# Optimization experiments

Hardware: AMD Instinct MI355X
Metric: run time of the kernel (lower is better)

Reference implementation:

```python
import jax, jax.numpy as jnp
import numpy as np

B, C, H, W = 32, 3, 128, 128
NMIX = 10  # 10 logistic mixture components -> 100 param channels for RGB


def setup_inputs() -> dict:
    key = jax.random.key(0)
    k1, k2 = jax.random.split(key)
    samples = jax.random.uniform(k1, (B, C, H, W), dtype=jnp.float32)  # pixel values in [0,1]
    params = jax.random.normal(k2, (B, 10 * NMIX, H, W), dtype=jnp.float32)  # PixelCNN output params
    return {"samples": samples, "params": params}


def _discretized_mix_logistic_log_prob(x, l):
    # x: [B,H,W,3] in [-1,1]; l: [B,H,W,100]
    logit_probs = l[..., :NMIX]                                   # [B,H,W,NMIX]
    rest = l[..., NMIX:].reshape(l.shape[0], l.shape[1], l.shape[2], 3, 3 * NMIX)
    means = rest[..., :NMIX]                                      # [B,H,W,3,NMIX]
    log_scales = jnp.maximum(rest[..., NMIX:2 * NMIX], -7.0)
    coeffs = jnp.tanh(rest[..., 2 * NMIX:3 * NMIX])

    x0 = x[..., 0:1]  # [B,H,W,1]
    x1 = x[..., 1:2]
    m1 = means[..., 0, :]
    m2 = means[..., 1, :] + coeffs[..., 0, :] * x0
    m3 = means[..., 2, :] + coeffs[..., 1, :] * x0 + coeffs[..., 2, :] * x1
    means_c = jnp.stack([m1, m2, m3], axis=3)                     # [B,H,W,3,NMIX]

    xb = x[..., None]                                             # [B,H,W,3,1]
    centered = xb - means_c
    inv_stdv = jnp.exp(-log_scales)
    plus_in = inv_stdv * (centered + 1.0 / 255.0)
    min_in = inv_stdv * (centered - 1.0 / 255.0)
    cdf_plus = jax.nn.sigmoid(plus_in)
    cdf_min = jax.nn.sigmoid(min_in)
    log_cdf_plus = plus_in - jax.nn.softplus(plus_in)             # log CDF at left edge bin (x = -1)
    log_one_minus_cdf_min = -jax.nn.softplus(min_in)              # log(1-CDF) at right edge bin (x = 1)
    cdf_delta = cdf_plus - cdf_min
    mid_in = inv_stdv * centered
    log_pdf_mid = mid_in - log_scales - 2.0 * jax.nn.softplus(mid_in)

    inner = jnp.where(cdf_delta > 1e-5,
                      jnp.log(jnp.maximum(cdf_delta, 1e-12)),
                      log_pdf_mid - np.float32(np.log(127.5)))
    log_probs_ch = jnp.where(xb < -0.999, log_cdf_plus,
                             jnp.where(xb > 0.999, log_one_minus_cdf_min, inner))
    # sum over channels, mixture weights, logsumexp over mixtures
    log_probs = log_probs_ch.sum(axis=3) + jax.nn.log_softmax(logit_probs, axis=-1)
    return jax.scipy.special.logsumexp(log_probs, axis=-1).sum()


def reference(samples, params):
    # _PixelCNNDistribution.log_prob: rescale samples to [-1,1], evaluate
    # discretized mixture-of-logistics log-likelihood (= -discretized_mix_logistic_loss).
    x = jnp.transpose(samples * 2.0 - 1.0, (0, 2, 3, 1))  # NCHW -> NHWC
    l = jnp.transpose(params, (0, 2, 3, 1))
    return _discretized_mix_logistic_log_prob(x, l)
```

## Files before the change

### kernel.cpp

```cpp
#include <hip/hip_runtime.h>
#include <math.h>

#define HW 16384
#define HW2 8192
#define NMIX 10
#define NPIX (32 * HW)
#define NTHREADS (NPIX / 2)
#define NBLOCKS (NTHREADS / 256)

__device__ __forceinline__ float fexp(float x) { return __expf(x); }
__device__ __forceinline__ float flog(float x) { return __logf(x); }
__device__ __forceinline__ float frcp(float x) { return __builtin_amdgcn_rcpf(x); }

__device__ __forceinline__ float ftanh(float y) {
    float t = fexp(-2.0f * fabsf(y));
    float r = (1.0f - t) * frcp(1.0f + t);
    return (y >= 0.0f) ? r : -r;
}

__device__ __forceinline__ float channel_logprob(float x, float mean, float ls,
                                                 bool waveEdge) {
    const float INV255 = 0.00392156862745098f;
    const float LOG127_5 = 4.852030263919617f;
    float inv = fexp(-ls);
    float centered = x - mean;
    float plus_in = inv * (centered + INV255);
    float min_in  = inv * (centered - INV255);
    float mid_in  = inv * centered;

    float tp = fexp(-fabsf(plus_in));
    float rp = frcp(1.0f + tp);
    float sig_plus = (plus_in >= 0.0f) ? rp : tp * rp;

    float tm = fexp(-fabsf(min_in));
    float rm = frcp(1.0f + tm);
    float sig_min = (min_in >= 0.0f) ? rm : tm * rm;

    float cdf_delta = sig_plus - sig_min;

    float tmid = fexp(-fabsf(mid_in));
    float sp_mid = fmaxf(mid_in, 0.0f) + flog(1.0f + tmid);
    float log_pdf_mid = mid_in - ls - 2.0f * sp_mid;

    float r = (cdf_delta > 1e-5f) ? flog(fmaxf(cdf_delta, 1e-12f))
                                  : (log_pdf_mid - LOG127_5);
    if (waveEdge) {
        float sp_plus = fmaxf(plus_in, 0.0f) + flog(1.0f + tp);
        float sp_min  = fmaxf(min_in, 0.0f) + flog(1.0f + tm);
        float log_cdf_plus   = plus_in - sp_plus;
        float log_om_cdf_min = -sp_min;
        r = (x < -0.999f) ? log_cdf_plus
          : ((x > 0.999f) ? log_om_cdf_min : r);
    }
    return r;
}

__device__ __forceinline__ void lse_update(float& m, float& s, float v) {
    float d = v - m;
    float e = fexp(-fabsf(d));
    bool grow = (d > 0.0f);
    s = grow ? (s * e + 1.0f) : (s + e);
    m = grow ? v : m;
}

__global__ __launch_bounds__(256, 6) void pixelcnn_kernel(
    const float2* __restrict__ samples, const float2* __restrict__ params,
    float* __restrict__ out)
{
    int q  = blockIdx.x * blockDim.x + threadIdx.x;
    int b  = q >> 13;
    int hw = q & (HW2 - 1);

    const float2* sp = samples + (size_t)b * 3   * HW2 + hw;
    const float2* pp = params  + (size_t)b * 100 * HW2 + hw;

    float2 s0 = sp[0];
    float2 s1 = sp[HW2];
    float2 s2 = sp[2 * HW2];

    float x0[2] = {2.0f * s0.x - 1.0f, 2.0f * s0.y - 1.0f};
    float x1[2] = {2.0f * s1.x - 1.0f, 2.0f * s1.y - 1.0f};
    float x2[2] = {2.0f * s2.x - 1.0f, 2.0f * s2.y - 1.0f};

    bool edge = false;
    #pragma unroll
    for (int j = 0; j < 2; ++j)
        edge |= (fabsf(x0[j]) > 0.999f) | (fabsf(x1[j]) > 0.999f)
              | (fabsf(x2[j]) > 0.999f);
    bool waveEdge = (__ballot(edge) != 0ULL);

    float mr[2] = {-3.4e38f, -3.4e38f}, sr[2] = {0.0f, 0.0f};
    float ml[2] = {-3.4e38f, -3.4e38f}, sl[2] = {0.0f, 0.0f};

    #pragma unroll 1
    for (int k = 0; k < NMIX; ++k) {
        const float2* pk = pp + (size_t)k * HW2;
        float2 cur[10];
        #pragma unroll
        for (int f = 0; f < 10; ++f) cur[f] = pk[(size_t)(10 * f) * HW2];

        const float* logit = (const float*)&cur[0];
        const float* mean0 = (const float*)&cur[1];
        const float* lsc0  = (const float*)&cur[2];
        const float* cw0   = (const float*)&cur[3];
        const float* mean1 = (const float*)&cur[4];
        const float* lsc1  = (const float*)&cur[5];
        const float* cw1   = (const float*)&cur[6];
        const float* mean2 = (const float*)&cur[7];
        const float* lsc2  = (const float*)&cur[8];
        const float* cw2   = (const float*)&cur[9];

        #pragma unroll
        for (int j = 0; j < 2; ++j) {
            float ls0 = fmaxf(lsc0[j], -7.0f);
            float ls1 = fmaxf(lsc1[j], -7.0f);
            float ls2 = fmaxf(lsc2[j], -7.0f);
            float c0 = ftanh(cw0[j]);
            float c1 = ftanh(cw1[j]);
            float c2 = ftanh(cw2[j]);

            float m1 = mean0[j];
            float m2 = mean1[j] + c0 * x0[j];
            float m3 = mean2[j] + c1 * x0[j] + c2 * x1[j];

            float lp = channel_logprob(x0[j], m1, ls0, waveEdge)
                     + channel_logprob(x1[j], m2, ls1, waveEdge)
                     + channel_logprob(x2[j], m3, ls2, waveEdge);

            lse_update(mr[j], sr[j], lp + logit[j]);
            lse_update(ml[j], sl[j], logit[j]);
        }
    }

    float val = 0.0f;
    #pragma unroll
    for (int j = 0; j < 2; ++j)
        val += (mr[j] + flog(sr[j])) - (ml[j] + flog(sl[j]));

    #pragma unroll
    for (int off = 32; off > 0; off >>= 1)
        val += __shfl_down(val, off, 64);

    __shared__ float wsum[4];
    int lane = threadIdx.x & 63;
    int wid  = threadIdx.x >> 6;
    if (lane == 0) wsum[wid] = val;
    __syncthreads();
    if (threadIdx.x == 0) {
        float bsum = (wsum[0] + wsum[1]) + (wsum[2] + wsum[3]);
        atomicAdd(out, bsum);
    }
}

extern "C" void kernel_launch(void* const* d_in, const int* in_sizes, int n_in,
                              void* d_out, int out_size, void* d_ws, size_t ws_size,
                              hipStream_t stream) {
    const float2* samples = (const float2*)d_in[0];
    const float2* params  = (const float2*)d_in[1];
    float* out = (float*)d_out;

    hipMemsetAsync(out, 0, sizeof(float), stream);
    pixelcnn_kernel<<<NBLOCKS, 256, 0, stream>>>(samples, params, out);
}
```

Baseline: 295.7 us.

## Compute mixture likelihood in probability domain instead of log-sum-exp

Replaces the per-channel log-probabilities and the online log-sum-exp with direct probabilities. Channel probabilities are multiplied, weighted by exp(logit), summed over mixtures, and a single log is taken at the end. This removes most logs and the max-tracking exps per mixture, and drops the wave-level edge ballot by always evaluating the edge cases with sigmoid values. It also raises the launch-bounds occupancy hint from 6 to 8. The trade-off is numerical: products of small probabilities can underflow in fp32, and unshifted exp(logit) can overflow, which could yield -inf or inaccurate sums on less benign inputs.

```diff
diff --git a/kernel.cpp b/kernel.cpp
--- a/kernel.cpp
+++ b/kernel.cpp
@@ -18,11 +18,9 @@
     return (y >= 0.0f) ? r : -r;
 }
 
-__device__ __forceinline__ float channel_logprob(float x, float mean, float ls,
-                                                 bool waveEdge) {
-    const float INV255 = 0.00392156862745098f;
-    const float LOG127_5 = 4.852030263919617f;
-    float inv = fexp(-ls);
+__device__ __forceinline__ float channel_prob(float x, float mean, float inv) {
+    const float INV255   = 0.00392156862745098f;
+    const float RCP127_5 = 0.00784313725490196f;
     float centered = x - mean;
     float plus_in = inv * (centered + INV255);
     float min_in  = inv * (centered - INV255);
@@ -34,36 +32,21 @@
 
     float tm = fexp(-fabsf(min_in));
     float rm = frcp(1.0f + tm);
-    float sig_min = (min_in >= 0.0f) ? rm : tm * rm;
+    float sig_min    = (min_in >= 0.0f) ? rm : tm * rm;
+    float om_sig_min = (min_in >= 0.0f) ? tm * rm : rm;
 
     float cdf_delta = sig_plus - sig_min;
 
     float tmid = fexp(-fabsf(mid_in));
-    float sp_mid = fmaxf(mid_in, 0.0f) + flog(1.0f + tmid);
-    float log_pdf_mid = mid_in - ls - 2.0f * sp_mid;
+    float rmid = frcp(1.0f + tmid);
+    float p_fall = inv * tmid * rmid * rmid * RCP127_5;
 
-    float r = (cdf_delta > 1e-5f) ? flog(fmaxf(cdf_delta, 1e-12f))
-                                  : (log_pdf_mid - LOG127_5);
-    if (waveEdge) {
-        float sp_plus = fmaxf(plus_in, 0.0f) + flog(1.0f + tp);
-        float sp_min  = fmaxf(min_in, 0.0f) + flog(1.0f + tm);
-        float log_cdf_plus   = plus_in - sp_plus;
-        float log_om_cdf_min = -sp_min;
-        r = (x < -0.999f) ? log_cdf_plus
-          : ((x > 0.999f) ? log_om_cdf_min : r);
-    }
-    return r;
+    float p = (cdf_delta > 1e-5f) ? cdf_delta : p_fall;
+    p = (x < -0.999f) ? sig_plus : ((x > 0.999f) ? om_sig_min : p);
+    return p;
 }
 
-__device__ __forceinline__ void lse_update(float& m, float& s, float v) {
-    float d = v - m;
-    float e = fexp(-fabsf(d));
-    bool grow = (d > 0.0f);
-    s = grow ? (s * e + 1.0f) : (s + e);
-    m = grow ? v : m;
-}
-
-__global__ __launch_bounds__(256, 6) void pixelcnn_kernel(
+__global__ __launch_bounds__(256, 8) void pixelcnn_kernel(
     const float2* __restrict__ samples, const float2* __restrict__ params,
     float* __restrict__ out)
 {
@@ -82,15 +65,8 @@
     float x1[2] = {2.0f * s1.x - 1.0f, 2.0f * s1.y - 1.0f};
     float x2[2] = {2.0f * s2.x - 1.0f, 2.0f * s2.y - 1.0f};
 
-    bool edge = false;
-    #pragma unroll
-    for (int j = 0; j < 2; ++j)
-        edge |= (fabsf(x0[j]) > 0.999f) | (fabsf(x1[j]) > 0.999f)
-              | (fabsf(x2[j]) > 0.999f);
-    bool waveEdge = (__ballot(edge) != 0ULL);
-
-    float mr[2] = {-3.4e38f, -3.4e38f}, sr[2] = {0.0f, 0.0f};
-    float ml[2] = {-3.4e38f, -3.4e38f}, sl[2] = {0.0f, 0.0f};
+    float sum_r[2] = {0.0f, 0.0f};
+    float sum_l[2] = {0.0f, 0.0f};
 
     #pragma unroll 1
     for (int k = 0; k < NMIX; ++k) {
@@ -112,9 +88,9 @@
 
         #pragma unroll
         for (int j = 0; j < 2; ++j) {
-            float ls0 = fmaxf(lsc0[j], -7.0f);
-            float ls1 = fmaxf(lsc1[j], -7.0f);
-            float ls2 = fmaxf(lsc2[j], -7.0f);
+            float inv0 = fexp(-fmaxf(lsc0[j], -7.0f));
+            float inv1 = fexp(-fmaxf(lsc1[j], -7.0f));
+            float inv2 = fexp(-fmaxf(lsc2[j], -7.0f));
             float c0 = ftanh(cw0[j]);
             float c1 = ftanh(cw1[j]);
             float c2 = ftanh(cw2[j]);
@@ -123,19 +99,18 @@
             float m2 = mean1[j] + c0 * x0[j];
             float m3 = mean2[j] + c1 * x0[j] + c2 * x1[j];
 
-            float lp = channel_logprob(x0[j], m1, ls0, waveEdge)
-                     + channel_logprob(x1[j], m2, ls1, waveEdge)
-                     + channel_logprob(x2[j], m3, ls2, waveEdge);
+            float p = channel_prob(x0[j], m1, inv0)
+                    * channel_prob(x1[j], m2, inv1)
+                    * channel_prob(x2[j], m3, inv2);
 
-            lse_update(mr[j], sr[j], lp + logit[j]);
-            lse_update(ml[j], sl[j], logit[j]);
+            float el = fexp(logit[j]);
+            sum_r[j] += el * p;
+            sum_l[j] += el;
         }
     }
 
-    float val = 0.0f;
-    #pragma unroll
-    for (int j = 0; j < 2; ++j)
-        val += (mr[j] + flog(sr[j])) - (ml[j] + flog(sl[j]));
+    float val = flog(sum_r[0] * frcp(sum_l[0]))
+              + flog(sum_r[1] * frcp(sum_l[1]));
 
     #pragma unroll
     for (int off = 32; off > 0; off >>= 1)
```

Result: no change. 292.4 us (-1.1%).
